# Optimization experiments

Hardware: AMD Instinct MI355X
Metric: run time of the kernel (lower is better)

The kernel has to match this reference:

```python
import jax, jax.numpy as jnp
import numpy as np

N = 300000      # number of documents
F = 136         # LTR features (MSLR-style)
H1, H2 = 128, 64
NPAIRS = 23     # ceil(sqrt(random_pairs=500))
SIGMA = 1.0


def setup_inputs() -> dict:
    key = jax.random.key(0)
    ks = jax.random.split(key, 9)
    x = jax.random.normal(ks[0], (N, F), dtype=jnp.float32)
    W1 = jax.random.normal(ks[1], (F, H1), dtype=jnp.float32) * 0.08
    b1 = jnp.zeros((H1,), jnp.float32)
    W2 = jax.random.normal(ks[2], (H1, H2), dtype=jnp.float32) * 0.08
    b2 = jnp.zeros((H2,), jnp.float32)
    Wout = jax.random.normal(ks[3], (H2, 1), dtype=jnp.float32) * 0.08
    bout = jnp.zeros((1,), jnp.float32)
    target = jax.random.randint(ks[4], (N,), 0, 5).astype(jnp.float32)
    random_docs = jax.random.randint(ks[5], (NPAIRS,), 0, N, dtype=jnp.int32)
    return {"x": x, "W1": W1, "b1": b1, "W2": W2, "b2": b2,
            "Wout": Wout, "bout": bout, "target": target,
            "random_docs": random_docs}


def reference(x, W1, b1, W2, b2, Wout, bout, target, random_docs):
    # scoring network (dropout = eval-mode identity)
    h = jax.nn.relu(x @ W1 + b1)
    h = jax.nn.relu(h @ W2 + b2)
    scores = (h @ Wout + bout)[:, 0]              # [N]

    # LambdaRank pseudo-loss over sampled docs (faithful incl. original bugs)
    t = jax.lax.stop_gradient(target)             # labels are detached in torch code
    labels = t[random_docs]                       # [n]
    n = labels.shape[0]
    w = 1.0 / jnp.arange(1, n + 1, dtype=jnp.float32)   # ERR rank weights 1/r
    # ERR(swap(x,y)) - ERR(orig) = (labels[y]-labels[x]) * (w[x]-w[y])
    absD = jnp.abs((labels[None, :] - labels[:, None]) * (w[:, None] - w[None, :]))  # [n,n]
    # z_j = s_i bug => calc_p == 0.5 always => lambda_ij = sigma*(0.5*(1-S) - 0.5)
    S = jnp.sign(labels[:, None] - labels[None, :])
    lam = SIGMA * (0.5 * (1.0 - S) - 0.5)
    # skip when sampled doc indices are equal (i == j on doc ids, not positions)
    mask = (random_docs[:, None] != random_docs[None, :]).astype(jnp.float32)
    # lambda_i / delta_i never reset across outer loop -> running cumulative sums
    cumL = jnp.cumsum(jnp.sum(lam * mask, axis=1))
    cumD = jnp.cumsum(jnp.sum(absD * mask, axis=1))
    s = scores[random_docs]                       # [n]
    loss = jnp.sum(cumL * cumD * s)
    return loss.reshape(1)
```

## Files before the change

kernel.cpp:

```cpp
#include <hip/hip_runtime.h>

#define NDOCS 23
#define FDIM 136
#define H1DIM 128
#define H2DIM 64
#define SIGMA 1.0f
#define NTHREADS 1024
#define G1 8
#define F_PER_G 17
#define G2 16
#define I_PER_G 8
#define XT_PITCH 24
#define H1T_PITCH 24

__global__ __launch_bounds__(NTHREADS) void lambdarank_loss_kernel(
    const float* __restrict__ x,
    const float* __restrict__ W1,
    const float* __restrict__ b1,
    const float* __restrict__ W2,
    const float* __restrict__ b2,
    const float* __restrict__ Wout,
    const float* __restrict__ bout,
    const float* __restrict__ target,
    const int*   __restrict__ docs,
    float* __restrict__ out)
{
    __shared__ float s_part[G1 * NDOCS * H1DIM];
    __shared__ float s_xT[FDIM * XT_PITCH];
    __shared__ float s_h1T[H1DIM * H1T_PITCH];
    __shared__ int   s_docs[NDOCS];
    __shared__ float s_labels[NDOCS];
    __shared__ float s_score[NDOCS];
    __shared__ float s_rowL[NDOCS];
    __shared__ float s_rowD[NDOCS];

    const int tid = threadIdx.x;

    int dd = 0;
    if (tid < 64) dd = docs[tid < NDOCS ? tid : 0];

    const int j1 = tid & (H1DIM - 1);
    const int g1 = tid >> 7;
    float w1r[F_PER_G];
    #pragma unroll
    for (int ff = 0; ff < F_PER_G; ++ff)
        w1r[ff] = W1[(g1 * F_PER_G + ff) * H1DIM + j1];

    const int j2 = tid & (H2DIM - 1);
    const int g2 = tid >> 6;
    float w2r[I_PER_G];
    #pragma unroll
    for (int ii = 0; ii < I_PER_G; ++ii)
        w2r[ii] = W2[(g2 * I_PER_G + ii) * H2DIM + j2];

    const float b1r   = b1[j1];
    const float b2r   = b2[j2];
    const float woutr = Wout[j2];
    const float boutr = bout[0];

    if (tid < NDOCS) s_docs[tid] = dd;
    __syncthreads();

    float lb = 0.0f;
    if (tid < 64) lb = target[dd];
    if (tid < NDOCS * (FDIM / 4)) {
        const int q = tid / NDOCS;
        const int k = tid - q * NDOCS;
        const float4 v = *reinterpret_cast<const float4*>(
            &x[(long long)s_docs[k] * FDIM + q * 4]);
        s_xT[(q * 4 + 0) * XT_PITCH + k] = v.x;
        s_xT[(q * 4 + 1) * XT_PITCH + k] = v.y;
        s_xT[(q * 4 + 2) * XT_PITCH + k] = v.z;
        s_xT[(q * 4 + 3) * XT_PITCH + k] = v.w;
    }
    if (tid < NDOCS) s_labels[tid] = lb;
    __syncthreads();

    {
        float acc[NDOCS];
        #pragma unroll
        for (int k = 0; k < NDOCS; ++k) acc[k] = 0.0f;
        #pragma unroll
        for (int ff = 0; ff < F_PER_G; ++ff) {
            const int f = g1 * F_PER_G + ff;
            alignas(16) float xv[XT_PITCH];
            #pragma unroll
            for (int q = 0; q < XT_PITCH / 4; ++q)
                *reinterpret_cast<float4*>(&xv[q * 4]) =
                    *reinterpret_cast<const float4*>(&s_xT[f * XT_PITCH + q * 4]);
            #pragma unroll
            for (int k = 0; k < NDOCS; ++k)
                acc[k] = fmaf(xv[k], w1r[ff], acc[k]);
        }
        #pragma unroll
        for (int k = 0; k < NDOCS; ++k)
            s_part[(g1 * NDOCS + k) * H1DIM + j1] = acc[k];
    }
    __syncthreads();

    #pragma unroll
    for (int m = 0; m < 3; ++m) {
        const int idx = tid + m * NTHREADS;
        if (idx < NDOCS * H1DIM) {
            const int k = idx >> 7;
            const int j = idx & (H1DIM - 1);
            float a = b1r;
            #pragma unroll
            for (int g = 0; g < G1; ++g)
                a += s_part[(g * NDOCS + k) * H1DIM + j];
            s_h1T[j * H1T_PITCH + k] = fmaxf(a, 0.0f);
        }
    }
    __syncthreads();

    {
        float acc[NDOCS];
        #pragma unroll
        for (int k = 0; k < NDOCS; ++k) acc[k] = 0.0f;
        #pragma unroll
        for (int ii = 0; ii < I_PER_G; ++ii) {
            const int i = g2 * I_PER_G + ii;
            alignas(16) float hv[H1T_PITCH];
            #pragma unroll
            for (int q = 0; q < H1T_PITCH / 4; ++q)
                *reinterpret_cast<float4*>(&hv[q * 4]) =
                    *reinterpret_cast<const float4*>(&s_h1T[i * H1T_PITCH + q * 4]);
            #pragma unroll
            for (int k = 0; k < NDOCS; ++k)
                acc[k] = fmaf(hv[k], w2r[ii], acc[k]);
        }
        #pragma unroll
        for (int k = 0; k < NDOCS; ++k)
            s_part[(g2 * NDOCS + k) * H2DIM + j2] = acc[k];
    }
    __syncthreads();

    #pragma unroll
    for (int m = 0; m < 2; ++m) {
        const int idx = tid + m * NTHREADS;
        float c = 0.0f;
        if (idx < NDOCS * H2DIM) {
            const int k = idx >> 6;
            const int i = idx & (H2DIM - 1);
            float a = b2r;
            #pragma unroll
            for (int g = 0; g < G2; ++g)
                a += s_part[(g * NDOCS + k) * H2DIM + i];
            c = fmaxf(a, 0.0f) * woutr;
        }
        #pragma unroll
        for (int off = 32; off > 0; off >>= 1)
            c += __shfl_down(c, off, 64);
        if ((tid & 63) == 0 && idx < NDOCS * H2DIM)
            s_score[idx >> 6] = c + boutr;
    }

    if (tid >= 512 && tid < 512 + NDOCS) {
        const int i  = tid - 512;
        const float li = s_labels[i];
        const float wi = 1.0f / (float)(i + 1);
        const int   di = s_docs[i];
        float rl = 0.0f, rd = 0.0f;
        for (int j = 0; j < NDOCS; ++j) {
            if (s_docs[j] == di) continue;
            const float lj = s_labels[j];
            const float wj = 1.0f / (float)(j + 1);
            const float dl = li - lj;
            const float S  = (dl > 0.0f) ? 1.0f : ((dl < 0.0f) ? -1.0f : 0.0f);
            rl += SIGMA * (0.5f * (1.0f - S) - 0.5f);
            rd += fabsf((lj - li) * (wi - wj));
        }
        s_rowL[i] = rl;
        s_rowD[i] = rd;
    }
    __syncthreads();

    if (tid == 0) {
        float cl = 0.0f, cd = 0.0f, loss = 0.0f;
        for (int i = 0; i < NDOCS; ++i) {
            cl += s_rowL[i];
            cd += s_rowD[i];
            loss += cl * cd * s_score[i];
        }
        out[0] = loss;
    }
}

extern "C" void kernel_launch(void* const* d_in, const int* in_sizes, int n_in,
                              void* d_out, int out_size, void* d_ws, size_t ws_size,
                              hipStream_t stream) {
    const float* x      = (const float*)d_in[0];
    const float* W1     = (const float*)d_in[1];
    const float* b1     = (const float*)d_in[2];
    const float* W2     = (const float*)d_in[3];
    const float* b2     = (const float*)d_in[4];
    const float* Wout   = (const float*)d_in[5];
    const float* bout   = (const float*)d_in[6];
    const float* target = (const float*)d_in[7];
    const int*   docs   = (const int*)d_in[8];
    float* out = (float*)d_out;

    hipLaunchKernelGGL(lambdarank_loss_kernel, dim3(1), dim3(NTHREADS), 0, stream,
                       x, W1, b1, W2, b2, Wout, bout, target, docs, out);
}
```

Measured before the change: 17.29 us.

## Halve block to 512 threads, widen per-thread work, and share docs via shuffles

The single-block kernel now runs 512 threads instead of 1024. Each wave computes two H1 columns per lane and 16 W2 rows per group, so the number of partial-sum groups in layer 2 drops from 16 to 8. Doc ids and labels are broadcast with wave shuffles instead of shared memory, which removes one __syncthreads and the shared staging arrays. The cost is more registers per thread (two accumulator sets of 23 each) and fewer threads to hide latency, with the h1T pitch changed to 28.

```diff
diff --git a/kernel.cpp b/kernel.cpp
--- a/kernel.cpp
+++ b/kernel.cpp
@@ -5,15 +5,15 @@
 #define H1DIM 128
 #define H2DIM 64
 #define SIGMA 1.0f
-#define NTHREADS 1024
+#define NT 512
 #define G1 8
-#define F_PER_G 17
-#define G2 16
-#define I_PER_G 8
+#define FPG 17
+#define G2 8
+#define IPG 16
 #define XT_PITCH 24
-#define H1T_PITCH 24
-
-__global__ __launch_bounds__(NTHREADS) void lambdarank_loss_kernel(
+#define H1T_PITCH 28
+
+__global__ __launch_bounds__(NT, 2) void lambdarank_loss_kernel(
     const float* __restrict__ x,
     const float* __restrict__ W1,
     const float* __restrict__ b1,
@@ -28,83 +28,84 @@
     __shared__ float s_part[G1 * NDOCS * H1DIM];
     __shared__ float s_xT[FDIM * XT_PITCH];
     __shared__ float s_h1T[H1DIM * H1T_PITCH];
-    __shared__ int   s_docs[NDOCS];
-    __shared__ float s_labels[NDOCS];
     __shared__ float s_score[NDOCS];
     __shared__ float s_rowL[NDOCS];
     __shared__ float s_rowD[NDOCS];
 
-    const int tid = threadIdx.x;
-
-    int dd = 0;
-    if (tid < 64) dd = docs[tid < NDOCS ? tid : 0];
-
-    const int j1 = tid & (H1DIM - 1);
-    const int g1 = tid >> 7;
-    float w1r[F_PER_G];
-    #pragma unroll
-    for (int ff = 0; ff < F_PER_G; ++ff)
-        w1r[ff] = W1[(g1 * F_PER_G + ff) * H1DIM + j1];
-
-    const int j2 = tid & (H2DIM - 1);
-    const int g2 = tid >> 6;
-    float w2r[I_PER_G];
-    #pragma unroll
-    for (int ii = 0; ii < I_PER_G; ++ii)
-        w2r[ii] = W2[(g2 * I_PER_G + ii) * H2DIM + j2];
-
-    const float b1r   = b1[j1];
-    const float b2r   = b2[j2];
-    const float woutr = Wout[j2];
+    const int tid  = threadIdx.x;
+    const int lane = tid & 63;
+    const int wv   = tid >> 6;
+
+    int dd = docs[lane < NDOCS ? lane : 0];
+
+    float w1a[FPG], w1b[FPG];
+    #pragma unroll
+    for (int ff = 0; ff < FPG; ++ff) {
+        w1a[ff] = W1[(wv * FPG + ff) * H1DIM + lane];
+        w1b[ff] = W1[(wv * FPG + ff) * H1DIM + lane + 64];
+    }
+    float w2r[IPG];
+    #pragma unroll
+    for (int ii = 0; ii < IPG; ++ii)
+        w2r[ii] = W2[(wv * IPG + ii) * H2DIM + lane];
+    const float b1a   = b1[lane];
+    const float b1b   = b1[lane + 64];
+    const float b2r   = b2[lane];
+    const float woutr = Wout[lane];
     const float boutr = bout[0];
 
-    if (tid < NDOCS) s_docs[tid] = dd;
-    __syncthreads();
-
     float lb = 0.0f;
-    if (tid < 64) lb = target[dd];
-    if (tid < NDOCS * (FDIM / 4)) {
-        const int q = tid / NDOCS;
-        const int k = tid - q * NDOCS;
-        const float4 v = *reinterpret_cast<const float4*>(
-            &x[(long long)s_docs[k] * FDIM + q * 4]);
-        s_xT[(q * 4 + 0) * XT_PITCH + k] = v.x;
-        s_xT[(q * 4 + 1) * XT_PITCH + k] = v.y;
-        s_xT[(q * 4 + 2) * XT_PITCH + k] = v.z;
-        s_xT[(q * 4 + 3) * XT_PITCH + k] = v.w;
-    }
-    if (tid < NDOCS) s_labels[tid] = lb;
+    if (wv == 7 && lane < NDOCS) lb = target[dd];
+
+    #pragma unroll
+    for (int m = 0; m < 2; ++m) {
+        const int idx = tid + m * NT;
+        const int q   = idx / NDOCS;
+        const int kk  = idx - q * NDOCS;
+        const int dk  = __shfl(dd, kk, 64);
+        if (idx < NDOCS * (FDIM / 4)) {
+            const float4 v = *reinterpret_cast<const float4*>(
+                &x[(long long)dk * FDIM + q * 4]);
+            s_xT[(q * 4 + 0) * XT_PITCH + kk] = v.x;
+            s_xT[(q * 4 + 1) * XT_PITCH + kk] = v.y;
+            s_xT[(q * 4 + 2) * XT_PITCH + kk] = v.z;
+            s_xT[(q * 4 + 3) * XT_PITCH + kk] = v.w;
+        }
+    }
     __syncthreads();
 
     {
-        float acc[NDOCS];
-        #pragma unroll
-        for (int k = 0; k < NDOCS; ++k) acc[k] = 0.0f;
-        #pragma unroll
-        for (int ff = 0; ff < F_PER_G; ++ff) {
-            const int f = g1 * F_PER_G + ff;
+        float accA[NDOCS], accB[NDOCS];
+        #pragma unroll
+        for (int k = 0; k < NDOCS; ++k) { accA[k] = 0.0f; accB[k] = 0.0f; }
+        #pragma unroll
+        for (int ff = 0; ff < FPG; ++ff) {
+            const float* xr = &s_xT[(wv * FPG + ff) * XT_PITCH];
             alignas(16) float xv[XT_PITCH];
             #pragma unroll
             for (int q = 0; q < XT_PITCH / 4; ++q)
                 *reinterpret_cast<float4*>(&xv[q * 4]) =
-                    *reinterpret_cast<const float4*>(&s_xT[f * XT_PITCH + q * 4]);
-            #pragma unroll
-            for (int k = 0; k < NDOCS; ++k)
-                acc[k] = fmaf(xv[k], w1r[ff], acc[k]);
-        }
-        #pragma unroll
-        for (int k = 0; k < NDOCS; ++k)
-            s_part[(g1 * NDOCS + k) * H1DIM + j1] = acc[k];
-    }
-    __syncthreads();
-
-    #pragma unroll
-    for (int m = 0; m < 3; ++m) {
-        const int idx = tid + m * NTHREADS;
-        if (idx < NDOCS * H1DIM) {
-            const int k = idx >> 7;
-            const int j = idx & (H1DIM - 1);
-            float a = b1r;
+                    *reinterpret_cast<const float4*>(&xr[q * 4]);
+            #pragma unroll
+            for (int k = 0; k < NDOCS; ++k) {
+                accA[k] = fmaf(xv[k], w1a[ff], accA[k]);
+                accB[k] = fmaf(xv[k], w1b[ff], accB[k]);
+            }
+        }
+        #pragma unroll
+        for (int k = 0; k < NDOCS; ++k) {
+            s_part[(wv * NDOCS + k) * H1DIM + lane]      = accA[k];
+            s_part[(wv * NDOCS + k) * H1DIM + lane + 64] = accB[k];
+        }
+    }
+    __syncthreads();
+
+    #pragma unroll
+    for (int m = 0; m < 6; ++m) {
+        const int k = wv + 8 * (m >> 1);
+        const int j = lane + 64 * (m & 1);
+        if (k < NDOCS) {
+            float a = (m & 1) ? b1b : b1a;
             #pragma unroll
             for (int g = 0; g < G1; ++g)
                 a += s_part[(g * NDOCS + k) * H1DIM + j];
@@ -118,60 +119,59 @@
         #pragma unroll
         for (int k = 0; k < NDOCS; ++k) acc[k] = 0.0f;
         #pragma unroll
-        for (int ii = 0; ii < I_PER_G; ++ii) {
-            const int i = g2 * I_PER_G + ii;
-            alignas(16) float hv[H1T_PITCH];
-            #pragma unroll
-            for (int q = 0; q < H1T_PITCH / 4; ++q)
+        for (int ii = 0; ii < IPG; ++ii) {
+            const float* hr = &s_h1T[(wv * IPG + ii) * H1T_PITCH];
+            alignas(16) float hv[24];
+            #pragma unroll
+            for (int q = 0; q < 6; ++q)
                 *reinterpret_cast<float4*>(&hv[q * 4]) =
-                    *reinterpret_cast<const float4*>(&s_h1T[i * H1T_PITCH + q * 4]);
+                    *reinterpret_cast<const float4*>(&hr[q * 4]);
             #pragma unroll
             for (int k = 0; k < NDOCS; ++k)
                 acc[k] = fmaf(hv[k], w2r[ii], acc[k]);
         }
         #pragma unroll
         for (int k = 0; k < NDOCS; ++k)
-            s_part[(g2 * NDOCS + k) * H2DIM + j2] = acc[k];
-    }
-    __syncthreads();
-
-    #pragma unroll
-    for (int m = 0; m < 2; ++m) {
-        const int idx = tid + m * NTHREADS;
+            s_part[(wv * NDOCS + k) * H2DIM + lane] = acc[k];
+    }
+    __syncthreads();
+
+    #pragma unroll
+    for (int m = 0; m < 3; ++m) {
+        const int idx = tid + m * NT;
         float c = 0.0f;
         if (idx < NDOCS * H2DIM) {
             const int k = idx >> 6;
-            const int i = idx & (H2DIM - 1);
             float a = b2r;
             #pragma unroll
             for (int g = 0; g < G2; ++g)
-                a += s_part[(g * NDOCS + k) * H2DIM + i];
+                a += s_part[(g * NDOCS + k) * H2DIM + lane];
             c = fmaxf(a, 0.0f) * woutr;
         }
         #pragma unroll
         for (int off = 32; off > 0; off >>= 1)
             c += __shfl_down(c, off, 64);
-        if ((tid & 63) == 0 && idx < NDOCS * H2DIM)
+        if (lane == 0 && idx < NDOCS * H2DIM)
             s_score[idx >> 6] = c + boutr;
     }
 
-    if (tid >= 512 && tid < 512 + NDOCS) {
-        const int i  = tid - 512;
-        const float li = s_labels[i];
-        const float wi = 1.0f / (float)(i + 1);
-        const int   di = s_docs[i];
+    if (wv == 7 && lane < NDOCS) {
+        const float li = lb;
+        const float wi = 1.0f / (float)(lane + 1);
+        const int   di = dd;
         float rl = 0.0f, rd = 0.0f;
         for (int j = 0; j < NDOCS; ++j) {
-            if (s_docs[j] == di) continue;
-            const float lj = s_labels[j];
+            const int   dj = __shfl(dd, j, 64);
+            const float lj = __shfl(lb, j, 64);
+            if (dj == di) continue;
             const float wj = 1.0f / (float)(j + 1);
             const float dl = li - lj;
             const float S  = (dl > 0.0f) ? 1.0f : ((dl < 0.0f) ? -1.0f : 0.0f);
             rl += SIGMA * (0.5f * (1.0f - S) - 0.5f);
             rd += fabsf((lj - li) * (wi - wj));
         }
-        s_rowL[i] = rl;
-        s_rowD[i] = rd;
+        s_rowL[lane] = rl;
+        s_rowD[lane] = rd;
     }
     __syncthreads();
 
@@ -198,8 +198,8 @@
     const float* bout   = (const float*)d_in[6];
     const float* target = (const float*)d_in[7];
     const int*   docs   = (const int*)d_in[8];
-    float* out = (float*)d_out;
-
-    hipLaunchKernelGGL(lambdarank_loss_kernel, dim3(1), dim3(NTHREADS), 0, stream,
-                       x, W1, b1, W2, b2, Wout, bout, target, docs, out);
+    float* outp = (float*)d_out;
+
+    hipLaunchKernelGGL(lambdarank_loss_kernel, dim3(1), dim3(NT), 0, stream,
+                       x, W1, b1, W2, b2, Wout, bout, target, docs, outp);
 }
```

Result: faster. 15.44 us (-10.6%).
